# Performance work log

Hardware: AMD Instinct MI355X
Metric: run time of the kernel (lower is better)

Reference implementation:

```python
import jax, jax.numpy as jnp
import numpy as np

B, T, C = 8, 1024, 1024
H, HS = 16, 64            # n_head, head_size
K, STRIDE = 32, 16        # block_length, stride_length
WIN = 128                 # local_window_size
EPS = 1e-5


def _ln(z, w):
    m = jnp.mean(z, axis=-1, keepdims=True)
    v = jnp.var(z, axis=-1, keepdims=True)
    return (z - m) / jnp.sqrt(v + EPS) * w


def setup_inputs() -> dict:
    key = jax.random.key(0)
    ks = jax.random.split(key, 8)
    s = 0.02
    return {
        "x": jax.random.normal(ks[0], (B, T, C), jnp.float32),
        "c_attn_w": jax.random.normal(ks[1], (3 * C, C), jnp.float32) * s,
        "conv_w": jax.random.normal(ks[2], (HS, HS, K), jnp.float32) * s,
        "ln_comp_w": jnp.ones((HS,), jnp.float32),
        "ln_local_w": jnp.ones((C,), jnp.float32),
        "gate_w1": jax.random.normal(ks[3], (C, 2 * C), jnp.float32) * s,
        "gate_ln_w": jnp.ones((C,), jnp.float32),
        "gate_w2": jax.random.normal(ks[4], (2, C), jnp.float32) * s,
        "c_proj_w": jax.random.normal(ks[5], (C, C), jnp.float32) * s,
    }


def reference(x, c_attn_w, conv_w, ln_comp_w, ln_local_w, gate_w1, gate_ln_w, gate_w2, c_proj_w):
    qkv = jnp.einsum('btc,oc->bto', x, c_attn_w)          # [B,T,3C]
    q, k, v = jnp.split(qkv, 3, axis=-1)
    def heads(t):
        return t.reshape(B, T, H, HS).transpose(0, 2, 1, 3)  # [B,H,T,hs]
    q, k, v = heads(q), heads(k), heads(v)

    # CompressionMLP: Conv1d over time + LayerNorm(hs) + exact GELU
    def compress(t):
        xr = t.transpose(0, 1, 3, 2).reshape(B * H, HS, T)   # [B*H, hs, T]
        co = jax.lax.conv_general_dilated(
            xr, conv_w, window_strides=(STRIDE,), padding='VALID',
            dimension_numbers=('NCH', 'OIH', 'NCH'))          # [B*H, hs, NB]
        co = co.transpose(0, 2, 1)                            # [B*H, NB, hs]
        co = jax.nn.gelu(_ln(co, ln_comp_w), approximate=False)
        nb = co.shape[1]
        return co.reshape(B, H, nb, HS)

    kc = compress(k)
    vc = compress(v)
    NB = kc.shape[2]  # 63
    scale = 1.0 / np.sqrt(HS)

    ti = jnp.arange(T)
    band = (ti[None, :] <= ti[:, None]) & (ti[None, :] >= ti[:, None] - WIN)  # [T,T]
    s_loc = jnp.einsum('bhqd,bhkd->bhqk', q, k) * scale
    s_loc = jnp.where(band[None, None], s_loc, -jnp.inf)
    local_out = jnp.einsum('bhqk,bhkd->bhqd', jax.nn.softmax(s_loc, axis=-1), v)
    local_out = local_out.transpose(0, 2, 1, 3).reshape(B, T, C)
    local_norm = _ln(local_out, ln_local_w)

    # compressed-KV attention with block-causal mask: block j <= token i
    bj = jnp.arange(NB)
    cmask = bj[None, :] <= ti[:, None]                        # [T,NB]
    s_cmp = jnp.einsum('bhqd,bhkd->bhqk', q, kc) * scale
    s_cmp = jnp.where(cmask[None, None], s_cmp, -jnp.inf)
    comp_out = jnp.einsum('bhqk,bhkd->bhqd', jax.nn.softmax(s_cmp, axis=-1), vc)
    comp_out = comp_out.transpose(0, 2, 1, 3).reshape(B, T, C)

    # AttentionGating: last-token features -> Linear -> LN -> ReLU -> Linear -> softmax
    feats = jnp.concatenate([local_norm[:, -1, :], comp_out[:, -1, :]], axis=-1)  # [B,2C]
    h = jax.nn.relu(_ln(feats @ gate_w1.T, gate_ln_w))
    gates = jax.nn.softmax(h @ gate_w2.T, axis=-1)            # [B,2]

    combined = gates[:, None, 0:1] * local_norm + gates[:, None, 1:2] * comp_out
    y = jnp.einsum('btc,oc->bto', combined, c_proj_w)
    return y
```

## Files before the change

kernel.cpp:

```cpp
#include <hip/hip_runtime.h>
#include <cstdint>
#include <cmath>
#include <cstddef>

typedef unsigned int u32;
typedef unsigned short u16;
typedef __bf16 bf16x8 __attribute__((ext_vector_type(8)));
typedef float f32x4 __attribute__((ext_vector_type(4)));
typedef u32 u32x4 __attribute__((ext_vector_type(4)));
typedef u32 u32x2 __attribute__((ext_vector_type(2)));

#define DEV static __device__ __forceinline__

DEV float bflo(u32 u) { return __uint_as_float(u << 16); }
DEV float bfhi(u32 u) { return __uint_as_float(u & 0xffff0000u); }
DEV u16 f2bf(float f) {
  u32 u = __float_as_uint(f);
  u += 0x7fffu + ((u >> 16) & 1u);
  return (u16)(u >> 16);
}
DEV f32x4 unpack_bf4(u32x2 r) {
  return (f32x4){bflo(r[0]), bfhi(r[0]), bflo(r[1]), bfhi(r[1])};
}
DEV float wredsum(float v) {
#pragma unroll
  for (int o = 32; o; o >>= 1) v += __shfl_xor(v, o, 64);
  return v;
}

DEV void gload_lds16(const u16* g, u16* lds_base) {
  __builtin_amdgcn_global_load_lds((const __attribute__((address_space(1))) void*)g,
                                   (__attribute__((address_space(3))) void*)lds_base,
                                   16, 0, 0);
}

__global__ __launch_bounds__(256) void fused_cast(const float* __restrict__ x,
                                                  const float* __restrict__ aw,
                                                  const float* __restrict__ pw,
                                                  const float* __restrict__ cw,
                                                  u16* __restrict__ xb,
                                                  u16* __restrict__ wab,
                                                  u16* __restrict__ wpb,
                                                  u16* __restrict__ wcb,
                                                  u16* __restrict__ kcb,
                                                  u16* __restrict__ vcb) {
  const int blk = blockIdx.x;
  if (blk < 12288) {
    const float* src;
    u16* dst;
    int base;
    if (blk < 8192) { src = x; dst = xb; base = blk; }
    else if (blk < 11264) { src = aw; dst = wab; base = blk - 8192; }
    else { src = pw; dst = wpb; base = blk - 11264; }
    const size_t idx = ((size_t)base * 256 + threadIdx.x) * 4;
    const f32x4 v = *(const f32x4*)&src[idx];
    u32x2 r;
    r[0] = (u32)f2bf(v[0]) | ((u32)f2bf(v[1]) << 16);
    r[1] = (u32)f2bf(v[2]) | ((u32)f2bf(v[3]) << 16);
    *(u32x2*)&dst[idx] = r;
  } else if (blk < 12800) {
    const int idx = (blk - 12288) * 256 + threadIdx.x;
    const int o = idx >> 11;
    const int rest = idx & 2047;
    const int i = rest >> 5;
    const int kk = rest & 31;
    wcb[(o << 11) + (kk << 6) + i] = f2bf(cw[idx]);
  } else {
    for (int i = threadIdx.x; i < 8192; i += 256) {
      const int bh = i >> 6, d = i & 63;
      kcb[bh * 4096 + 63 * 64 + d] = 0;
      vcb[bh * 4096 + d * 64 + 63] = 0;
    }
  }
}

template <int OUT_BF16>
__global__ __launch_bounds__(256, 4) void gemm_bt(const u16* __restrict__ A,
                                                  const u16* __restrict__ Bm,
                                                  void* __restrict__ out,
                                                  int M, int N, int K) {
  __shared__ u16 As[128 * 64];
  __shared__ u16 Bs[128 * 64];
  const int tid = threadIdx.x;
  const int lane = tid & 63;
  const int w = tid >> 6;
  const int row0 = blockIdx.x * 128;
  const int col0 = blockIdx.y * 128;
  const int wm = (w >> 1) * 64, wn = (w & 1) * 64;
  const int lr = lane & 15, lq = lane >> 4;
  const int srow = lane >> 3;
  const int scol = ((lane & 7) ^ (srow & 7)) * 8;
  const int pgA = ((lq ^ (lr & 7)) * 8);

  f32x4 acc[4][4] = {};

  for (int k0 = 0; k0 < K; k0 += 64) {
    __syncthreads();
#pragma unroll
    for (int c = 0; c < 4; ++c) {
      const int base_r = w * 32 + c * 8;
      gload_lds16(&A[(size_t)(row0 + base_r + srow) * K + k0 + scol], &As[base_r * 64]);
      gload_lds16(&Bm[(size_t)(col0 + base_r + srow) * K + k0 + scol], &Bs[base_r * 64]);
    }
    __syncthreads();
#pragma unroll
    for (int ks = 0; ks < 2; ++ks) {
      const int pg = pgA ^ (ks << 5);
      bf16x8 af[4], bfr[4];
#pragma unroll
      for (int i = 0; i < 4; ++i) {
        af[i] = *(const bf16x8*)&As[(wm + i * 16 + lr) * 64 + pg];
        bfr[i] = *(const bf16x8*)&Bs[(wn + i * 16 + lr) * 64 + pg];
      }
#pragma unroll
      for (int i = 0; i < 4; ++i)
#pragma unroll
        for (int j = 0; j < 4; ++j)
          acc[i][j] = __builtin_amdgcn_mfma_f32_16x16x32_bf16(af[i], bfr[j], acc[i][j], 0, 0, 0);
    }
  }
#pragma unroll
  for (int i = 0; i < 4; ++i)
#pragma unroll
    for (int j = 0; j < 4; ++j)
#pragma unroll
      for (int rr = 0; rr < 4; ++rr) {
        const int gr = row0 + wm + i * 16 + lq * 4 + rr;
        const int gc = col0 + wn + j * 16 + lr;
        const float v = acc[i][j][rr];
        if (OUT_BF16)
          ((u16*)out)[(size_t)gr * N + gc] = f2bf(v);
        else
          ((float*)out)[(size_t)gr * N + gc] = v;
      }
}

__global__ __launch_bounds__(256) void compress_kernel(const u16* __restrict__ qkv,
                                                       const u16* __restrict__ Wc,
                                                       const float* __restrict__ ln_w,
                                                       u16* __restrict__ kcb,
                                                       u16* __restrict__ vcb) {
  __shared__ u16 As[2][32 * 128];
  __shared__ u16 Bs[2][64 * 128];
  __shared__ float Cs[32][65];
  const int tid = threadIdx.x;
  const int lane = tid & 63, w = tid >> 6;
  const int lr = lane & 15, lq = lane >> 4;
  const int r0 = blockIdx.x * 32;
  const int srcoff = 1024 + (int)blockIdx.y * 1024;

  size_t abase[2];
#pragma unroll
  for (int g2 = 0; g2 < 2; ++g2) {
    const int r = 8 * w + 4 * g2 + (lane >> 4);
    const int gr = r0 + r;
    const int bh = gr / 63;
    const int nb = gr - bh * 63;
    const int b = bh >> 4, h = bh & 15;
    const int jbit = (lane >> 3) & 1;
    const int icol = ((lane & 7) ^ (r & 7)) * 8;
    abase[g2] = (size_t)(b * 1024 + nb * 16 + jbit) * 3072 + srcoff + h * 64 + icol;
  }
  size_t bbase[4];
#pragma unroll
  for (int c = 0; c < 4; ++c) {
    const int rB = 16 * w + 4 * c + (lane >> 4);
    const int Lcol = (((lane & 7) ^ (rB & 7)) | (lane & 8)) * 8;
    bbase[c] = (size_t)rB * 2048 + Lcol;
  }

  auto stage = [&](int it, int bs) {
#pragma unroll
    for (int g2 = 0; g2 < 2; ++g2)
      gload_lds16(&qkv[abase[g2] + (size_t)it * 6144], &As[bs][(8 * w + 4 * g2) * 128]);
#pragma unroll
    for (int c = 0; c < 4; ++c)
      gload_lds16(&Wc[bbase[c] + (size_t)it * 128], &Bs[bs][(16 * w + 4 * c) * 128]);
  };

  const int rw = (w & 1) * 16;
  const int cw = (w >> 1) * 32;
  f32x4 acc[2] = {};

  stage(0, 0);
  for (int it = 0; it < 16; ++it) {
    const int cur = it & 1;
    __syncthreads();
    if (it < 15) stage(it + 1, cur ^ 1);
    const int rowA = rw + lr;
#pragma unroll
    for (int ks = 0; ks < 4; ++ks) {
      const int L = ks * 4 + lq;
      const int pgA = (((L & 7) ^ (rowA & 7)) | (L & 8)) * 8;
      const bf16x8 af = *(const bf16x8*)&As[cur][rowA * 128 + pgA];
#pragma unroll
      for (int j = 0; j < 2; ++j) {
        const int rowB = cw + j * 16 + lr;
        const int pgB = (((L & 7) ^ (rowB & 7)) | (L & 8)) * 8;
        const bf16x8 bfr = *(const bf16x8*)&Bs[cur][rowB * 128 + pgB];
        acc[j] = __builtin_amdgcn_mfma_f32_16x16x32_bf16(af, bfr, acc[j], 0, 0, 0);
      }
    }
  }
  __syncthreads();
#pragma unroll
  for (int j = 0; j < 2; ++j)
#pragma unroll
    for (int rr = 0; rr < 4; ++rr)
      Cs[rw + lq * 4 + rr][cw + j * 16 + lr] = acc[j][rr];
  __syncthreads();
  if (tid < 32) {
    const int gr2 = r0 + tid;
    const int bh2 = gr2 / 63;
    const int nb2 = gr2 - bh2 * 63;
    float s = 0.f, s2 = 0.f;
#pragma unroll 8
    for (int d = 0; d < 64; ++d) {
      const float xv = Cs[tid][d];
      s += xv;
      s2 += xv * xv;
    }
    const float m = s * (1.f / 64.f);
    const float inv = rsqrtf(s2 * (1.f / 64.f) - m * m + 1e-5f);
    if (blockIdx.y == 0) {
      const size_t gb = (size_t)bh2 * 4096 + nb2 * 64;
#pragma unroll 8
      for (int d = 0; d < 64; ++d) {
        const float z = (Cs[tid][d] - m) * inv * ln_w[d];
        kcb[gb + d] = f2bf(0.5f * z * (1.f + erff(z * 0.70710678118f)));
      }
    } else {
      const size_t gb = (size_t)bh2 * 4096 + nb2;
#pragma unroll 8
      for (int d = 0; d < 64; ++d) {
        const float z = (Cs[tid][d] - m) * inv * ln_w[d];
        vcb[gb + d * 64] = f2bf(0.5f * z * (1.f + erff(z * 0.70710678118f)));
      }
    }
  }
}

__global__ __launch_bounds__(256, 4) void attn_fused(const u16* __restrict__ qkv,
                                                     const u16* __restrict__ kcb,
                                                     const u16* __restrict__ vcb,
                                                     u16* __restrict__ loc,
                                                     u16* __restrict__ outc) {
  __shared__ __align__(16) char smem[53248];
  u16* Ks = (u16*)smem;
  u16* Ps = (u16*)smem;
  u16* Vt = (u16*)(smem + 27648);
  u16* Kc = (u16*)smem;
  u16* Vc = (u16*)(smem + 9216);
  u16* Pc = (u16*)(smem + 18432);
  const int bh = blockIdx.x;
  const int b = bh >> 4, h = bh & 15;
  const int i0 = blockIdx.y * 64;
  const int jbase = i0 - 128;
  const int tid = threadIdx.x;
  const int lane = tid & 63, w = tid >> 6;
  const int lr = lane & 15, lq = lane >> 4;

#pragma unroll
  for (int c = 0; c < 6; ++c) {
    const int lin = c * 256 + tid;
    const int s = lin >> 3, d0 = (lin & 7) * 8;
    const int j = jbase + s;
    u32x4 kval = {0, 0, 0, 0}, vval = {0, 0, 0, 0};
    if (j >= 0) {
      const size_t ro = (size_t)(b * 1024 + j) * 3072 + h * 64 + d0;
      kval = *(const u32x4*)&qkv[ro + 1024];
      vval = *(const u32x4*)&qkv[ro + 2048];
    }
    *(u32x4*)&Ks[s * 72 + d0] = kval;
    const int sg = (((s >> 3) ^ (lane & 7)) << 3) | (s & 7);
#pragma unroll
    for (int q = 0; q < 4; ++q) {
      Vt[(d0 + 2 * q) * 200 + sg] = (u16)(vval[q] & 0xffffu);
      Vt[(d0 + 2 * q + 1) * 200 + sg] = (u16)(vval[q] >> 16);
    }
  }
  bf16x8 qf[2];
  {
    const size_t qrow = (size_t)(b * 1024 + i0 + w * 16 + lr) * 3072 + h * 64;
#pragma unroll
    for (int ks = 0; ks < 2; ++ks) qf[ks] = *(const bf16x8*)&qkv[qrow + ks * 32 + lq * 8];
  }
  const size_t cb = (size_t)bh * 4096;
  u32x4 kcreg[2], vcreg[2];
#pragma unroll
  for (int c2 = 0; c2 < 2; ++c2) {
    const int i2 = c2 * 256 + tid;
    const size_t o2 = (size_t)(i2 >> 3) * 64 + (i2 & 7) * 8;
    kcreg[c2] = *(const u32x4*)&kcb[cb + o2];
    vcreg[c2] = *(const u32x4*)&vcb[cb + o2];
  }
  __syncthreads();

  f32x4 sa[9];
#pragma unroll
  for (int j9 = 0; j9 < 9; ++j9) sa[j9] = (f32x4){0.f, 0.f, 0.f, 0.f};
#pragma unroll
  for (int ks = 0; ks < 2; ++ks)
#pragma unroll
    for (int j9 = 0; j9 < 9; ++j9) {
      const int jt = w + j9;
      const bf16x8 kf = *(const bf16x8*)&Ks[(jt * 16 + lr) * 72 + ks * 32 + lq * 8];
      sa[j9] = __builtin_amdgcn_mfma_f32_16x16x32_bf16(qf[ks], kf, sa[j9], 0, 0, 0);
    }

  const float NINF = -__builtin_inff();
  float mx[4] = {NINF, NINF, NINF, NINF};
#pragma unroll
  for (int j9 = 0; j9 < 9; ++j9) {
    const int s = (w + j9) * 16 + lr;
#pragma unroll
    for (int rr = 0; rr < 4; ++rr) {
      const int qi = w * 16 + lq * 4 + rr;
      const bool valid = (jbase + s >= 0) && (s >= qi) && (s <= qi + 128);
      const float v = valid ? sa[j9][rr] * 0.125f : NINF;
      sa[j9][rr] = v;
      mx[rr] = fmaxf(mx[rr], v);
    }
  }
#pragma unroll
  for (int rr = 0; rr < 4; ++rr)
#pragma unroll
    for (int o = 1; o < 16; o <<= 1) mx[rr] = fmaxf(mx[rr], __shfl_xor(mx[rr], o, 64));
  float sum[4] = {0.f, 0.f, 0.f, 0.f};
#pragma unroll
  for (int j9 = 0; j9 < 9; ++j9)
#pragma unroll
    for (int rr = 0; rr < 4; ++rr) {
      const float p = __expf(sa[j9][rr] - mx[rr]);
      sa[j9][rr] = p;
      sum[rr] += p;
    }
#pragma unroll
  for (int rr = 0; rr < 4; ++rr) {
#pragma unroll
    for (int o = 1; o < 16; o <<= 1) sum[rr] += __shfl_xor(sum[rr], o, 64);
    sum[rr] = 1.0f / sum[rr];
  }
  __syncthreads();

#pragma unroll
  for (int j9 = 0; j9 < 9; ++j9) {
    const int jt = w + j9;
#pragma unroll
    for (int rr = 0; rr < 4; ++rr)
      Ps[(w * 16 + lq * 4 + rr) * 200 + jt * 16 + lr] = f2bf(sa[j9][rr] * sum[rr]);
  }
  {
    const int jz = (w == 0) ? 9 : (w == 1) ? 0 : (w == 2) ? 11 : 2;
#pragma unroll
    for (int rr = 0; rr < 4; ++rr) Ps[(w * 16 + lq * 4 + rr) * 200 + jz * 16 + lr] = 0;
  }
  asm volatile("" ::: "memory");

  const int W = (w >> 1) * 32;
  const int G0 = W >> 3;
  f32x4 oa[4];
#pragma unroll
  for (int jt = 0; jt < 4; ++jt) oa[jt] = (f32x4){0.f, 0.f, 0.f, 0.f};
#pragma unroll
  for (int ks = 0; ks < 5; ++ks) {
    const bf16x8 pf = *(const bf16x8*)&Ps[(w * 16 + lr) * 200 + W + ks * 32 + lq * 8];
#pragma unroll
    for (int jt = 0; jt < 4; ++jt) {
      const int rl = jt * 16 + lr;
      const int g = G0 + ks * 4 + lq;
      const bf16x8 vf = *(const bf16x8*)&Vt[rl * 200 + ((g ^ (rl >> 3)) << 3)];
      oa[jt] = __builtin_amdgcn_mfma_f32_16x16x32_bf16(pf, vf, oa[jt], 0, 0, 0);
    }
  }
#pragma unroll
  for (int jt = 0; jt < 4; ++jt)
#pragma unroll
    for (int rr = 0; rr < 4; ++rr)
      loc[(size_t)(b * 1024 + i0 + w * 16 + lq * 4 + rr) * 1024 + h * 64 + jt * 16 + lr] =
          f2bf(oa[jt][rr]);

  __syncthreads();
#pragma unroll
  for (int c2 = 0; c2 < 2; ++c2) {
    const int i2 = c2 * 256 + tid;
    const int r2 = i2 >> 3, o2 = (i2 & 7) * 8;
    *(u32x4*)&Kc[r2 * 72 + o2] = kcreg[c2];
    *(u32x4*)&Vc[r2 * 72 + o2] = vcreg[c2];
  }
  __syncthreads();

  f32x4 ca[4];
#pragma unroll
  for (int j = 0; j < 4; ++j) ca[j] = (f32x4){0.f, 0.f, 0.f, 0.f};
#pragma unroll
  for (int ks = 0; ks < 2; ++ks)
#pragma unroll
    for (int j = 0; j < 4; ++j) {
      const bf16x8 kf = *(const bf16x8*)&Kc[(j * 16 + lr) * 72 + ks * 32 + lq * 8];
      ca[j] = __builtin_amdgcn_mfma_f32_16x16x32_bf16(qf[ks], kf, ca[j], 0, 0, 0);
    }
  float mc[4] = {NINF, NINF, NINF, NINF};
#pragma unroll
  for (int j = 0; j < 4; ++j) {
    const int s = j * 16 + lr;
#pragma unroll
    for (int rr = 0; rr < 4; ++rr) {
      const int i = i0 + w * 16 + lq * 4 + rr;
      const bool valid = (s <= i) && (s < 63);
      const float v = valid ? ca[j][rr] * 0.125f : NINF;
      ca[j][rr] = v;
      mc[rr] = fmaxf(mc[rr], v);
    }
  }
#pragma unroll
  for (int rr = 0; rr < 4; ++rr)
#pragma unroll
    for (int o = 1; o < 16; o <<= 1) mc[rr] = fmaxf(mc[rr], __shfl_xor(mc[rr], o, 64));
  float sc[4] = {0.f, 0.f, 0.f, 0.f};
#pragma unroll
  for (int j = 0; j < 4; ++j)
#pragma unroll
    for (int rr = 0; rr < 4; ++rr) {
      const float p = __expf(ca[j][rr] - mc[rr]);
      ca[j][rr] = p;
      sc[rr] += p;
    }
#pragma unroll
  for (int rr = 0; rr < 4; ++rr) {
#pragma unroll
    for (int o = 1; o < 16; o <<= 1) sc[rr] += __shfl_xor(sc[rr], o, 64);
    sc[rr] = 1.0f / sc[rr];
  }
#pragma unroll
  for (int j = 0; j < 4; ++j)
#pragma unroll
    for (int rr = 0; rr < 4; ++rr)
      Pc[(w * 16 + lq * 4 + rr) * 72 + j * 16 + lr] = f2bf(ca[j][rr] * sc[rr]);
  asm volatile("" ::: "memory");

  f32x4 co[4];
#pragma unroll
  for (int jt = 0; jt < 4; ++jt) co[jt] = (f32x4){0.f, 0.f, 0.f, 0.f};
#pragma unroll
  for (int ks = 0; ks < 2; ++ks) {
    const bf16x8 pf = *(const bf16x8*)&Pc[(w * 16 + lr) * 72 + ks * 32 + lq * 8];
#pragma unroll
    for (int jt = 0; jt < 4; ++jt) {
      const bf16x8 vf = *(const bf16x8*)&Vc[(jt * 16 + lr) * 72 + ks * 32 + lq * 8];
      co[jt] = __builtin_amdgcn_mfma_f32_16x16x32_bf16(pf, vf, co[jt], 0, 0, 0);
    }
  }
#pragma unroll
  for (int jt = 0; jt < 4; ++jt)
#pragma unroll
    for (int rr = 0; rr < 4; ++rr)
      outc[(size_t)(b * 1024 + i0 + w * 16 + lq * 4 + rr) * 1024 + h * 64 + jt * 16 + lr] =
          f2bf(co[jt][rr]);
}

__global__ __launch_bounds__(256) void gate_gemv(const u16* __restrict__ locb,
                                                 const u16* __restrict__ compb,
                                                 const float* __restrict__ lnw,
                                                 const float* __restrict__ w1,
                                                 float* __restrict__ hraw) {
  __shared__ float sm[8], sinv[8];
  const int tid = threadIdx.x;
  const int w = tid >> 6, lane = tid & 63;
  for (int bb = w; bb < 8; bb += 4) {
    const u16* rp = &locb[((size_t)bb * 1024 + 1023) * 1024 + lane * 16];
    const u32x4 a0 = *(const u32x4*)rp;
    const u32x4 a1 = *(const u32x4*)(rp + 8);
    float s = 0.f, s2 = 0.f;
#pragma unroll
    for (int q = 0; q < 4; ++q) {
      const float x0 = bflo(a0[q]), x1 = bfhi(a0[q]);
      const float x2 = bflo(a1[q]), x3 = bfhi(a1[q]);
      s += x0 + x1 + x2 + x3;
      s2 += x0 * x0 + x1 * x1 + x2 * x2 + x3 * x3;
    }
    s = wredsum(s);
    s2 = wredsum(s2);
    if (!lane) {
      const float m = s * (1.f / 1024.f);
      sm[bb] = m;
      sinv[bb] = rsqrtf(s2 * (1.f / 1024.f) - m * m + 1e-5f);
    }
  }
  __syncthreads();

  const int o = blockIdx.x * 4 + w;
  const float* wr = &w1[(size_t)o * 2048];
  float acc[8] = {};
#pragma unroll
  for (int it = 0; it < 4; ++it) {
    const int c = (it * 64 + lane) * 4;
    const f32x4 wv = *(const f32x4*)&wr[c];
    const f32x4 lw = *(const f32x4*)&lnw[c];
#pragma unroll
    for (int b = 0; b < 8; ++b) {
      const f32x4 xv = unpack_bf4(*(const u32x2*)&locb[((size_t)b * 1024 + 1023) * 1024 + c]);
      const float mb = sm[b], ib = sinv[b];
      acc[b] += ((xv[0] - mb) * ib * lw[0]) * wv[0] + ((xv[1] - mb) * ib * lw[1]) * wv[1] +
                ((xv[2] - mb) * ib * lw[2]) * wv[2] + ((xv[3] - mb) * ib * lw[3]) * wv[3];
    }
  }
#pragma unroll
  for (int it = 4; it < 8; ++it) {
    const int c = (it * 64 + lane) * 4;
    const f32x4 wv = *(const f32x4*)&wr[c];
    const int c2 = c - 1024;
#pragma unroll
    for (int b = 0; b < 8; ++b) {
      const f32x4 fv = unpack_bf4(*(const u32x2*)&compb[((size_t)b * 1024 + 1023) * 1024 + c2]);
      acc[b] += fv[0] * wv[0] + fv[1] * wv[1] + fv[2] * wv[2] + fv[3] * wv[3];
    }
  }
#pragma unroll
  for (int b = 0; b < 8; ++b) acc[b] = wredsum(acc[b]);
  if (lane == 0) {
#pragma unroll
    for (int b = 0; b < 8; ++b) hraw[b * 1024 + o] = acc[b];
  }
}

__global__ __launch_bounds__(256) void gate_fin(const float* __restrict__ hraw,
                                                const float* __restrict__ lnw,
                                                const float* __restrict__ w2,
                                                float* __restrict__ gates) {
  const int b = blockIdx.x, tid = threadIdx.x;
  const f32x4 v = *(const f32x4*)&hraw[(size_t)b * 1024 + tid * 4];
  float s = v[0] + v[1] + v[2] + v[3];
  float s2 = v[0] * v[0] + v[1] * v[1] + v[2] * v[2] + v[3] * v[3];
  s = wredsum(s);
  s2 = wredsum(s2);
  __shared__ float rs[4], rs2[4];
  const int w = tid >> 6, lane = tid & 63;
  if (!lane) { rs[w] = s; rs2[w] = s2; }
  __syncthreads();
  s = rs[0] + rs[1] + rs[2] + rs[3];
  s2 = rs2[0] + rs2[1] + rs2[2] + rs2[3];
  const float m = s * (1.f / 1024.f);
  const float inv = rsqrtf(s2 * (1.f / 1024.f) - m * m + 1e-5f);
  float p0 = 0.f, p1 = 0.f;
#pragma unroll
  for (int k = 0; k < 4; ++k) {
    float hh = (v[k] - m) * inv * lnw[tid * 4 + k];
    hh = fmaxf(hh, 0.f);
    p0 += hh * w2[tid * 4 + k];
    p1 += hh * w2[1024 + tid * 4 + k];
  }
  p0 = wredsum(p0);
  p1 = wredsum(p1);
  __syncthreads();
  if (!lane) { rs[w] = p0; rs2[w] = p1; }
  __syncthreads();
  if (tid == 0) {
    const float l0 = rs[0] + rs[1] + rs[2] + rs[3];
    const float l1 = rs2[0] + rs2[1] + rs2[2] + rs2[3];
    const float mm = fmaxf(l0, l1);
    const float e0 = __expf(l0 - mm), e1 = __expf(l1 - mm);
    const float iv = 1.f / (e0 + e1);
    gates[b * 2] = e0 * iv;
    gates[b * 2 + 1] = e1 * iv;
  }
}

__global__ __launch_bounds__(256) void combine_ln_cast(const u16* __restrict__ locb,
                                                       const u16* __restrict__ compb,
                                                       const float* __restrict__ lnw,
                                                       const float* __restrict__ gates,
                                                       u16* __restrict__ outb) {
  const int w = threadIdx.x >> 6, lane = threadIdx.x & 63;
  const int row = blockIdx.x * 4 + w;
  const size_t base = (size_t)row * 1024 + lane * 16;
  const u32x4 a0 = *(const u32x4*)&locb[base];
  const u32x4 a1 = *(const u32x4*)&locb[base + 8];
  float xv[16];
#pragma unroll
  for (int q = 0; q < 4; ++q) {
    xv[2 * q] = bflo(a0[q]);
    xv[2 * q + 1] = bfhi(a0[q]);
    xv[8 + 2 * q] = bflo(a1[q]);
    xv[8 + 2 * q + 1] = bfhi(a1[q]);
  }
  float s = 0.f, s2 = 0.f;
#pragma unroll
  for (int k = 0; k < 16; ++k) {
    s += xv[k];
    s2 += xv[k] * xv[k];
  }
  s = wredsum(s);
  s2 = wredsum(s2);
  const float m = s * (1.f / 1024.f);
  const float inv = rsqrtf(s2 * (1.f / 1024.f) - m * m + 1e-5f);
  const int b = row >> 10;
  const float g0 = gates[2 * b], g1 = gates[2 * b + 1];
  const u32x4 c0 = *(const u32x4*)&compb[base];
  const u32x4 c1 = *(const u32x4*)&compb[base + 8];
  const f32x4 lw0 = *(const f32x4*)&lnw[lane * 16];
  const f32x4 lw1 = *(const f32x4*)&lnw[lane * 16 + 4];
  const f32x4 lw2 = *(const f32x4*)&lnw[lane * 16 + 8];
  const f32x4 lw3 = *(const f32x4*)&lnw[lane * 16 + 12];
  u32x4 r0, r1;
#pragma unroll
  for (int q = 0; q < 4; ++q) {
    const float lwa = (q < 2) ? lw0[2 * q] : lw1[2 * q - 4];
    const float lwb = (q < 2) ? lw0[2 * q + 1] : lw1[2 * q - 3];
    const float lwc = (q < 2) ? lw2[2 * q] : lw3[2 * q - 4];
    const float lwd = (q < 2) ? lw2[2 * q + 1] : lw3[2 * q - 3];
    const float o0 = g0 * ((xv[2 * q] - m) * inv * lwa) + g1 * bflo(c0[q]);
    const float o1 = g0 * ((xv[2 * q + 1] - m) * inv * lwb) + g1 * bfhi(c0[q]);
    const float o2 = g0 * ((xv[8 + 2 * q] - m) * inv * lwc) + g1 * bflo(c1[q]);
    const float o3 = g0 * ((xv[8 + 2 * q + 1] - m) * inv * lwd) + g1 * bfhi(c1[q]);
    r0[q] = (u32)f2bf(o0) | ((u32)f2bf(o1) << 16);
    r1[q] = (u32)f2bf(o2) | ((u32)f2bf(o3) << 16);
  }
  *(u32x4*)&outb[base] = r0;
  *(u32x4*)&outb[base + 8] = r1;
}

extern "C" void kernel_launch(void* const* d_in, const int* in_sizes, int n_in,
                              void* d_out, int out_size, void* d_ws, size_t ws_size,
                              hipStream_t stream) {
  const float* x = (const float*)d_in[0];
  const float* c_attn_w = (const float*)d_in[1];
  const float* conv_w = (const float*)d_in[2];
  const float* ln_comp_w = (const float*)d_in[3];
  const float* ln_local_w = (const float*)d_in[4];
  const float* gate_w1 = (const float*)d_in[5];
  const float* gate_ln_w = (const float*)d_in[6];
  const float* gate_w2 = (const float*)d_in[7];
  const float* c_proj_w = (const float*)d_in[8];
  float* y = (float*)d_out;

  char* ws = (char*)d_ws;
  size_t off = 0;
  auto alloc = [&](size_t bytes) -> void* {
    void* p = ws + off;
    off += (bytes + 255) & ~(size_t)255;
    return p;
  };
  u16* qkvb = (u16*)alloc((size_t)8192 * 3072 * 2);
  u16* xb = (u16*)alloc((size_t)8192 * 1024 * 2);
  u16* wab = (u16*)alloc((size_t)3072 * 1024 * 2);
  u16* wpb = (u16*)alloc((size_t)1024 * 1024 * 2);
  u16* wcb = (u16*)alloc((size_t)64 * 2048 * 2);
  u16* kcb = (u16*)alloc((size_t)128 * 4096 * 2);
  u16* vcb = (u16*)alloc((size_t)128 * 4096 * 2);
  u16* locb = (u16*)alloc((size_t)8192 * 1024 * 2);
  u16* compb = (u16*)alloc((size_t)8192 * 1024 * 2);
  float* hraw = (float*)alloc((size_t)8192 * 4);
  float* gates = (float*)alloc(64);
  u16* combb = (u16*)alloc((size_t)8192 * 1024 * 2);

  fused_cast<<<12801, 256, 0, stream>>>(x, c_attn_w, c_proj_w, conv_w, xb, wab, wpb, wcb, kcb,
                                        vcb);

  gemm_bt<1><<<dim3(64, 24), 256, 0, stream>>>(xb, wab, qkvb, 8192, 3072, 1024);

  compress_kernel<<<dim3(252, 2), 256, 0, stream>>>(qkvb, wcb, ln_comp_w, kcb, vcb);

  attn_fused<<<dim3(128, 16), 256, 0, stream>>>(qkvb, kcb, vcb, locb, compb);

  gate_gemv<<<256, 256, 0, stream>>>(locb, compb, ln_local_w, gate_w1, hraw);
  gate_fin<<<8, 256, 0, stream>>>(hraw, gate_ln_w, gate_w2, gates);

  combine_ln_cast<<<2048, 256, 0, stream>>>(locb, compb, ln_local_w, gates, combb);

  gemm_bt<0><<<dim3(64, 8), 256, 0, stream>>>(combb, wpb, y, 8192, 1024, 1024);
}
```

Before: 272.7 us.

## Load local K tile via direct global-to-LDS with XOR swizzle; fold gate_fin into combine

The attention kernel now brings the local K tile into shared memory with gload_lds16 direct global-to-LDS loads into an unpadded, XOR-swizzled layout instead of register round-trips into a padded layout. This cuts register traffic and LDS footprint, and the MFMA K reads use the matching swizzle. Separately, the tiny gate_fin kernel is removed and each combine block recomputes the gate LayerNorm, ReLU, second linear and softmax from hraw, saving one launch and its dependency. In exchange, every combine block does the redundant gate reduction, and rows with j<0 load clamped row 0 instead of zeros, which relies on masking downstream.

```diff
diff --git a/kernel.cpp b/kernel.cpp
--- a/kernel.cpp
+++ b/kernel.cpp
@@ -245,10 +245,10 @@
                                                      const u16* __restrict__ vcb,
                                                      u16* __restrict__ loc,
                                                      u16* __restrict__ outc) {
-  __shared__ __align__(16) char smem[53248];
+  __shared__ __align__(16) char smem[51200];
   u16* Ks = (u16*)smem;
   u16* Ps = (u16*)smem;
-  u16* Vt = (u16*)(smem + 27648);
+  u16* Vt = (u16*)(smem + 25600);
   u16* Kc = (u16*)smem;
   u16* Vc = (u16*)(smem + 9216);
   u16* Pc = (u16*)(smem + 18432);
@@ -259,19 +259,23 @@
   const int tid = threadIdx.x;
   const int lane = tid & 63, w = tid >> 6;
   const int lr = lane & 15, lq = lane >> 4;
-
+  const int srow = lane >> 3;
+  const int scol = ((lane & 7) ^ srow) * 8;
+
+#pragma unroll
+  for (int g = 0; g < 6; ++g) {
+    const int rb = (w * 6 + g) * 8;
+    int jc = jbase + rb + srow;
+    jc = jc < 0 ? 0 : jc;
+    gload_lds16(&qkv[(size_t)(b * 1024 + jc) * 3072 + 1024 + h * 64 + scol], &Ks[rb * 64]);
+  }
 #pragma unroll
   for (int c = 0; c < 6; ++c) {
     const int lin = c * 256 + tid;
     const int s = lin >> 3, d0 = (lin & 7) * 8;
     const int j = jbase + s;
-    u32x4 kval = {0, 0, 0, 0}, vval = {0, 0, 0, 0};
-    if (j >= 0) {
-      const size_t ro = (size_t)(b * 1024 + j) * 3072 + h * 64 + d0;
-      kval = *(const u32x4*)&qkv[ro + 1024];
-      vval = *(const u32x4*)&qkv[ro + 2048];
-    }
-    *(u32x4*)&Ks[s * 72 + d0] = kval;
+    u32x4 vval = {0, 0, 0, 0};
+    if (j >= 0) vval = *(const u32x4*)&qkv[(size_t)(b * 1024 + j) * 3072 + 2048 + h * 64 + d0];
     const int sg = (((s >> 3) ^ (lane & 7)) << 3) | (s & 7);
 #pragma unroll
     for (int q = 0; q < 4; ++q) {
@@ -304,7 +308,8 @@
 #pragma unroll
     for (int j9 = 0; j9 < 9; ++j9) {
       const int jt = w + j9;
-      const bf16x8 kf = *(const bf16x8*)&Ks[(jt * 16 + lr) * 72 + ks * 32 + lq * 8];
+      const bf16x8 kf =
+          *(const bf16x8*)&Ks[(jt * 16 + lr) * 64 + (((ks * 4 + lq) ^ (lr & 7)) * 8)];
       sa[j9] = __builtin_amdgcn_mfma_f32_16x16x32_bf16(qf[ks], kf, sa[j9], 0, 0, 0);
     }
 
@@ -524,54 +529,55 @@
   }
 }
 
-__global__ __launch_bounds__(256) void gate_fin(const float* __restrict__ hraw,
-                                                const float* __restrict__ lnw,
-                                                const float* __restrict__ w2,
-                                                float* __restrict__ gates) {
-  const int b = blockIdx.x, tid = threadIdx.x;
-  const f32x4 v = *(const f32x4*)&hraw[(size_t)b * 1024 + tid * 4];
-  float s = v[0] + v[1] + v[2] + v[3];
-  float s2 = v[0] * v[0] + v[1] * v[1] + v[2] * v[2] + v[3] * v[3];
-  s = wredsum(s);
-  s2 = wredsum(s2);
+__global__ __launch_bounds__(256) void combine_ln_cast(const u16* __restrict__ locb,
+                                                       const u16* __restrict__ compb,
+                                                       const float* __restrict__ lnw,
+                                                       const float* __restrict__ glnw,
+                                                       const float* __restrict__ w2,
+                                                       const float* __restrict__ hraw,
+                                                       u16* __restrict__ outb) {
+  const int tid = threadIdx.x;
+  const int w = tid >> 6, lane = tid & 63;
+  const int b = (blockIdx.x * 4) >> 10;
+
   __shared__ float rs[4], rs2[4];
-  const int w = tid >> 6, lane = tid & 63;
-  if (!lane) { rs[w] = s; rs2[w] = s2; }
-  __syncthreads();
-  s = rs[0] + rs[1] + rs[2] + rs[3];
-  s2 = rs2[0] + rs2[1] + rs2[2] + rs2[3];
-  const float m = s * (1.f / 1024.f);
-  const float inv = rsqrtf(s2 * (1.f / 1024.f) - m * m + 1e-5f);
-  float p0 = 0.f, p1 = 0.f;
-#pragma unroll
-  for (int k = 0; k < 4; ++k) {
-    float hh = (v[k] - m) * inv * lnw[tid * 4 + k];
-    hh = fmaxf(hh, 0.f);
-    p0 += hh * w2[tid * 4 + k];
-    p1 += hh * w2[1024 + tid * 4 + k];
-  }
-  p0 = wredsum(p0);
-  p1 = wredsum(p1);
-  __syncthreads();
-  if (!lane) { rs[w] = p0; rs2[w] = p1; }
-  __syncthreads();
-  if (tid == 0) {
+  const f32x4 hv = *(const f32x4*)&hraw[(size_t)b * 1024 + tid * 4];
+  {
+    float s = hv[0] + hv[1] + hv[2] + hv[3];
+    float s2 = hv[0] * hv[0] + hv[1] * hv[1] + hv[2] * hv[2] + hv[3] * hv[3];
+    s = wredsum(s);
+    s2 = wredsum(s2);
+    if (!lane) { rs[w] = s; rs2[w] = s2; }
+  }
+  __syncthreads();
+  float g0, g1;
+  {
+    const float s = rs[0] + rs[1] + rs[2] + rs[3];
+    const float s2 = rs2[0] + rs2[1] + rs2[2] + rs2[3];
+    const float m = s * (1.f / 1024.f);
+    const float inv = rsqrtf(s2 * (1.f / 1024.f) - m * m + 1e-5f);
+    float p0 = 0.f, p1 = 0.f;
+#pragma unroll
+    for (int k = 0; k < 4; ++k) {
+      float hh = (hv[k] - m) * inv * glnw[tid * 4 + k];
+      hh = fmaxf(hh, 0.f);
+      p0 += hh * w2[tid * 4 + k];
+      p1 += hh * w2[1024 + tid * 4 + k];
+    }
+    p0 = wredsum(p0);
+    p1 = wredsum(p1);
+    __syncthreads();
+    if (!lane) { rs[w] = p0; rs2[w] = p1; }
+    __syncthreads();
     const float l0 = rs[0] + rs[1] + rs[2] + rs[3];
     const float l1 = rs2[0] + rs2[1] + rs2[2] + rs2[3];
     const float mm = fmaxf(l0, l1);
     const float e0 = __expf(l0 - mm), e1 = __expf(l1 - mm);
     const float iv = 1.f / (e0 + e1);
-    gates[b * 2] = e0 * iv;
-    gates[b * 2 + 1] = e1 * iv;
-  }
-}
-
-__global__ __launch_bounds__(256) void combine_ln_cast(const u16* __restrict__ locb,
-                                                       const u16* __restrict__ compb,
-                                                       const float* __restrict__ lnw,
-                                                       const float* __restrict__ gates,
-                                                       u16* __restrict__ outb) {
-  const int w = threadIdx.x >> 6, lane = threadIdx.x & 63;
+    g0 = e0 * iv;
+    g1 = e1 * iv;
+  }
+
   const int row = blockIdx.x * 4 + w;
   const size_t base = (size_t)row * 1024 + lane * 16;
   const u32x4 a0 = *(const u32x4*)&locb[base];
@@ -594,8 +600,6 @@
   s2 = wredsum(s2);
   const float m = s * (1.f / 1024.f);
   const float inv = rsqrtf(s2 * (1.f / 1024.f) - m * m + 1e-5f);
-  const int b = row >> 10;
-  const float g0 = gates[2 * b], g1 = gates[2 * b + 1];
   const u32x4 c0 = *(const u32x4*)&compb[base];
   const u32x4 c1 = *(const u32x4*)&compb[base + 8];
   const f32x4 lw0 = *(const f32x4*)&lnw[lane * 16];
@@ -651,7 +655,6 @@
   u16* locb = (u16*)alloc((size_t)8192 * 1024 * 2);
   u16* compb = (u16*)alloc((size_t)8192 * 1024 * 2);
   float* hraw = (float*)alloc((size_t)8192 * 4);
-  float* gates = (float*)alloc(64);
   u16* combb = (u16*)alloc((size_t)8192 * 1024 * 2);
 
   fused_cast<<<12801, 256, 0, stream>>>(x, c_attn_w, c_proj_w, conv_w, xb, wab, wpb, wcb, kcb,
@@ -664,9 +667,9 @@
   attn_fused<<<dim3(128, 16), 256, 0, stream>>>(qkvb, kcb, vcb, locb, compb);
 
   gate_gemv<<<256, 256, 0, stream>>>(locb, compb, ln_local_w, gate_w1, hraw);
-  gate_fin<<<8, 256, 0, stream>>>(hraw, gate_ln_w, gate_w2, gates);
-
-  combine_ln_cast<<<2048, 256, 0, stream>>>(locb, compb, ln_local_w, gates, combb);
+
+  combine_ln_cast<<<2048, 256, 0, stream>>>(locb, compb, ln_local_w, gate_ln_w, gate_w2, hraw,
+                                            combb);
 
   gemm_bt<0><<<dim3(64, 8), 256, 0, stream>>>(combb, wpb, y, 8192, 1024, 1024);
 }
```

Measured after the change: 268.8 us (median of 2 runs). No clear change (-1.4%).
